# Optimization experiments

Hardware: AMD Instinct MI355X
Metric: run time of the kernel (lower is better)

## Reference

```python
import jax, jax.numpy as jnp
import numpy as np

N_NODES = 50000
N_EDGES = 800000
IN_FEATS = 64
HIDDEN = 64
NUM_CLASSES = 32


def _graph_conv(x, src, dst, W, b, n_nodes):
    # DGL GraphConv, norm='both', allow_zero_in_degree=True:
    # out = D_in^{-1/2} * (A^T @ (D_out^{-1/2} * x)) @ W + b, degrees clamped to >=1
    e = src.shape[0]
    ones = jnp.ones((e,), dtype=x.dtype)
    out_deg = jax.ops.segment_sum(ones, src, num_segments=n_nodes)
    in_deg = jax.ops.segment_sum(ones, dst, num_segments=n_nodes)
    norm_src = jax.lax.rsqrt(jnp.maximum(out_deg, 1.0))[:, None]
    norm_dst = jax.lax.rsqrt(jnp.maximum(in_deg, 1.0))[:, None]
    h = x * norm_src                                   # [N, d]
    agg = jax.ops.segment_sum(h[src], dst, num_segments=n_nodes)  # gather+scatter over edges
    return (agg * norm_dst) @ W + b


def setup_inputs() -> dict:
    key = jax.random.key(0)
    k1, k2, k3, k4, k5 = jax.random.split(key, 5)
    features = jax.random.normal(k1, (N_NODES, IN_FEATS), dtype=jnp.float32)
    src = jax.random.randint(k2, (N_EDGES,), 0, N_NODES, dtype=jnp.int32)
    dst = jax.random.randint(k3, (N_EDGES,), 0, N_NODES, dtype=jnp.int32)
    W1 = jax.random.normal(k4, (IN_FEATS, HIDDEN), dtype=jnp.float32) * (1.0 / np.sqrt(IN_FEATS))
    b1 = jnp.zeros((HIDDEN,), dtype=jnp.float32)
    W2 = jax.random.normal(k5, (HIDDEN, NUM_CLASSES), dtype=jnp.float32) * (1.0 / np.sqrt(HIDDEN))
    b2 = jnp.zeros((NUM_CLASSES,), dtype=jnp.float32)
    return {"features": features, "src": src, "dst": dst,
            "W1": W1, "b1": b1, "W2": W2, "b2": b2}


def reference(features, src, dst, W1, b1, W2, b2) -> jnp.ndarray:
    n = features.shape[0]
    h = jax.nn.relu(_graph_conv(features, src, dst, W1, b1, n))
    out = _graph_conv(h, src, dst, W2, b2, n)
    # single canonical etype -> mean over one-element stack is identity
    return out
```

## Files before the change

kernel.cpp:

```cpp
#include <hip/hip_runtime.h>
#include <hip/hip_bf16.h>

#define N_NODES 50000
#define N_EDGES 800000
#define F 64
#define C 32
#define CAP 48

#define NPB   800
#define EPB   1000
#define NBUCK 196
#define SEGCAP 5120

#define G1_BLOCKS   2048
#define GOUT_BLOCKS 2048
#define GY_BLOCKS   2048

static __device__ __forceinline__ float bflo(int u) {
    return __uint_as_float(((unsigned)u) << 16);
}
static __device__ __forceinline__ float bfhi(int u) {
    return __uint_as_float(((unsigned)u) & 0xffff0000u);
}
static __device__ __forceinline__ unsigned short f2bf(float f) {
    __hip_bfloat16 h = __float2bfloat16(f);
    return *reinterpret_cast<unsigned short*>(&h);
}

__global__ void part_fused_kernel(const int* __restrict__ src, const int* __restrict__ dst,
                                  int* __restrict__ gseg,
                                  int* __restrict__ edge_d, unsigned char* __restrict__ edge_s) {
    __shared__ int hd[4][NBUCK], hs[4][NBUCK];
    int t = threadIdx.x;
    int w = t >> 6;
    for (int i = t; i < 4 * NBUCK; i += 256) {
        (&hd[0][0])[i] = 0;
        (&hs[0][0])[i] = 0;
    }
    __syncthreads();
    int b0 = blockIdx.x * EPB;
    const int4* s4 = reinterpret_cast<const int4*>(src + b0);
    const int4* d4 = reinterpret_cast<const int4*>(dst + b0);
    for (int i = t; i < EPB / 4; i += 256) {
        int4 dv = d4[i];
        int4 sv = s4[i];
        atomicAdd(&hd[w][dv.x >> 8], 1); atomicAdd(&hd[w][dv.y >> 8], 1);
        atomicAdd(&hd[w][dv.z >> 8], 1); atomicAdd(&hd[w][dv.w >> 8], 1);
        atomicAdd(&hs[w][sv.x >> 8], 1); atomicAdd(&hs[w][sv.y >> 8], 1);
        atomicAdd(&hs[w][sv.z >> 8], 1); atomicAdd(&hs[w][sv.w >> 8], 1);
    }
    __syncthreads();
    if (t < NBUCK) {
        int c0 = hd[0][t], c1 = hd[1][t], c2 = hd[2][t], c3 = hd[3][t];
        int base = t * SEGCAP + atomicAdd(&gseg[t], c0 + c1 + c2 + c3);
        hd[0][t] = base;
        hd[1][t] = base + c0;
        hd[2][t] = base + c0 + c1;
        hd[3][t] = base + c0 + c1 + c2;
        c0 = hs[0][t]; c1 = hs[1][t]; c2 = hs[2][t]; c3 = hs[3][t];
        base = t * SEGCAP + atomicAdd(&gseg[NBUCK + t], c0 + c1 + c2 + c3);
        hs[0][t] = base;
        hs[1][t] = base + c0;
        hs[2][t] = base + c0 + c1;
        hs[3][t] = base + c0 + c1 + c2;
    }
    __syncthreads();
    for (int i = t; i < EPB / 4; i += 256) {
        int4 dv = d4[i];
        int4 sv = s4[i];
        int p;
        p = atomicAdd(&hd[w][dv.x >> 8], 1); edge_d[p] = ((dv.x & 255) << 16) | sv.x;
        p = atomicAdd(&hd[w][dv.y >> 8], 1); edge_d[p] = ((dv.y & 255) << 16) | sv.y;
        p = atomicAdd(&hd[w][dv.z >> 8], 1); edge_d[p] = ((dv.z & 255) << 16) | sv.z;
        p = atomicAdd(&hd[w][dv.w >> 8], 1); edge_d[p] = ((dv.w & 255) << 16) | sv.w;
        p = atomicAdd(&hs[w][sv.x >> 8], 1); edge_s[p] = (unsigned char)(sv.x & 255);
        p = atomicAdd(&hs[w][sv.y >> 8], 1); edge_s[p] = (unsigned char)(sv.y & 255);
        p = atomicAdd(&hs[w][sv.z >> 8], 1); edge_s[p] = (unsigned char)(sv.z & 255);
        p = atomicAdd(&hs[w][sv.w >> 8], 1); edge_s[p] = (unsigned char)(sv.w & 255);
    }
}

__global__ void bucket_build_kernel(const int* __restrict__ edge_d,
                                    const unsigned char* __restrict__ edge_s,
                                    const int* __restrict__ gseg,
                                    unsigned short* __restrict__ csr,
                                    float4* __restrict__ meta) {
    __shared__ int cur[256];
    __shared__ int hsm[256];
    int t = threadIdx.x;
    int bucket = blockIdx.x;
    cur[t] = 0;
    hsm[t] = 0;
    __syncthreads();
    int lend = gseg[bucket];           if (lend > SEGCAP) lend = SEGCAP;
    int lens = gseg[NBUCK + bucket];   if (lens > SEGCAP) lens = SEGCAP;
    int lo = bucket * SEGCAP;
    for (int i = lo + t; i < lo + lend; i += 256) {
        int pd = edge_d[i];
        int dlow = pd >> 16;
        int s = pd & 0xFFFF;
        int pos = atomicAdd(&cur[dlow], 1);
        if (pos < CAP)
            csr[(size_t)(bucket * 256 + dlow) * CAP + pos] = (unsigned short)s;
    }
    for (int i = lo + t; i < lo + lens; i += 256) {
        atomicAdd(&hsm[edge_s[i]], 1);
    }
    __syncthreads();
    int node = bucket * 256 + t;
    if (node < N_NODES) {
        int c = cur[t] < CAP ? cur[t] : CAP;
        float4 m;
        m.x = rsqrtf(fmaxf((float)c, 1.0f));
        m.y = rsqrtf(fmaxf((float)hsm[t], 1.0f));
        m.z = __int_as_float(c);
        m.w = 0.f;
        meta[node] = m;
    }
}

__global__ void gemm_y_kernel(const float* __restrict__ x,
                              const float4* __restrict__ meta,
                              const float* __restrict__ W,
                              __hip_bfloat16* __restrict__ y) {
    __shared__ float sW[F * F];
    __shared__ float srow[16][F];
    int t = threadIdx.x;
    for (int i = t; i < F * F; i += 256) sW[i] = W[i];
    int j = t & 63;
    int w = t >> 6;
    for (int tile = blockIdx.x; tile < N_NODES / 16; tile += GY_BLOCKS) {
        int base = tile * 16;
        __syncthreads();
        for (int r = w; r < 16; r += 4) srow[r][j] = x[(size_t)(base + r) * F + j];
        __syncthreads();
        float a0 = 0, a1 = 0, a2 = 0, a3 = 0;
#pragma unroll
        for (int k = 0; k < F; k++) {
            float wv = sW[k * F + j];
            a0 += srow[w * 4 + 0][k] * wv;
            a1 += srow[w * 4 + 1][k] * wv;
            a2 += srow[w * 4 + 2][k] * wv;
            a3 += srow[w * 4 + 3][k] * wv;
        }
        int n0 = base + w * 4;
        y[(size_t)(n0 + 0) * F + j] = __float2bfloat16(a0 * meta[n0 + 0].y);
        y[(size_t)(n0 + 1) * F + j] = __float2bfloat16(a1 * meta[n0 + 1].y);
        y[(size_t)(n0 + 2) * F + j] = __float2bfloat16(a2 * meta[n0 + 2].y);
        y[(size_t)(n0 + 3) * F + j] = __float2bfloat16(a3 * meta[n0 + 3].y);
    }
}

__global__ void gather64_gemv_kernel(const __hip_bfloat16* __restrict__ y,
                                     const unsigned short* __restrict__ csr,
                                     const float4* __restrict__ meta,
                                     const float* __restrict__ b1,
                                     const float* __restrict__ W2,
                                     __hip_bfloat16* __restrict__ gt) {
    __shared__ float sW[F * C];
    int t = threadIdx.x;
    for (int i = t; i < F * C; i += 256) sW[i] = W2[i];
    __syncthreads();
    int w    = t >> 6;
    int lane = t & 63;
    int g  = lane >> 3;
    int fo = (lane & 7) * 8;
    int j    = lane & 31;
    int half = lane >> 5;
    const float4 b1a = *reinterpret_cast<const float4*>(b1 + fo);
    const float4 b1b = *reinterpret_cast<const float4*>(b1 + fo + 4);
    const unsigned short* ytab = reinterpret_cast<const unsigned short*>(y);
    const int STRIDE = G1_BLOCKS * 4;

    int node = blockIdx.x * 4 + w;
    float4 pm = meta[node];
    const unsigned short* prow = csr + (size_t)node * CAP;
    int pr0 = prow[g], pr1 = prow[8 + g], pr2 = prow[16 + g];

    while (node < N_NODES) {
        float nd = pm.x, ns = pm.y;
        int n = __float_as_int(pm.z);
        int r0 = pr0, r1 = pr1, r2 = pr2;
        int nxt = node + STRIDE;
        int pf = (nxt < N_NODES) ? nxt : node;

        int ss0 = (g      < n) ? r0 : 0;  float m0 = (g      < n) ? 1.f : 0.f;
        int ss1 = (8  + g < n) ? r1 : 0;  float m1 = (8  + g < n) ? 1.f : 0.f;
        int ss2 = (16 + g < n) ? r2 : 0;  float m2 = (16 + g < n) ? 1.f : 0.f;

        const int4 v0 = *reinterpret_cast<const int4*>(ytab + (size_t)ss0 * F + fo);
        const int4 v1 = *reinterpret_cast<const int4*>(ytab + (size_t)ss1 * F + fo);
        const int4 v2 = *reinterpret_cast<const int4*>(ytab + (size_t)ss2 * F + fo);

        pm = meta[pf];
        const unsigned short* nrow = csr + (size_t)pf * CAP;
        pr0 = nrow[g]; pr1 = nrow[8 + g]; pr2 = nrow[16 + g];

        float a0, a1, a2, a3, a4, a5, a6, a7;
        a0 = m0 * bflo(v0.x); a1 = m0 * bfhi(v0.x);
        a2 = m0 * bflo(v0.y); a3 = m0 * bfhi(v0.y);
        a4 = m0 * bflo(v0.z); a5 = m0 * bfhi(v0.z);
        a6 = m0 * bflo(v0.w); a7 = m0 * bfhi(v0.w);

#define G1_ACC(vv, mm)                                                        \
        a0 = fmaf(mm, bflo(vv.x), a0); a1 = fmaf(mm, bfhi(vv.x), a1);         \
        a2 = fmaf(mm, bflo(vv.y), a2); a3 = fmaf(mm, bfhi(vv.y), a3);         \
        a4 = fmaf(mm, bflo(vv.z), a4); a5 = fmaf(mm, bfhi(vv.z), a5);         \
        a6 = fmaf(mm, bflo(vv.w), a6); a7 = fmaf(mm, bfhi(vv.w), a7);
        G1_ACC(v1, m1)
        G1_ACC(v2, m2)

        if (__builtin_expect(n > 24, 0)) {
            const unsigned short* row = csr + (size_t)node * CAP;
            int r3 = row[24 + g], r4 = row[32 + g], r5 = row[40 + g];
            int ss3 = (24 + g < n) ? r3 : 0;  float m3 = (24 + g < n) ? 1.f : 0.f;
            int ss4 = (32 + g < n) ? r4 : 0;  float m4 = (32 + g < n) ? 1.f : 0.f;
            int ss5 = (40 + g < n) ? r5 : 0;  float m5 = (40 + g < n) ? 1.f : 0.f;
            const int4 v3 = *reinterpret_cast<const int4*>(ytab + (size_t)ss3 * F + fo);
            const int4 v4 = *reinterpret_cast<const int4*>(ytab + (size_t)ss4 * F + fo);
            const int4 v5 = *reinterpret_cast<const int4*>(ytab + (size_t)ss5 * F + fo);
            G1_ACC(v3, m3)
            G1_ACC(v4, m4)
            G1_ACC(v5, m5)
        }
#undef G1_ACC

#define G1_RED(mk)                                                           \
        a0 += __shfl_xor(a0, mk); a1 += __shfl_xor(a1, mk);                  \
        a2 += __shfl_xor(a2, mk); a3 += __shfl_xor(a3, mk);                  \
        a4 += __shfl_xor(a4, mk); a5 += __shfl_xor(a5, mk);                  \
        a6 += __shfl_xor(a6, mk); a7 += __shfl_xor(a7, mk);
        G1_RED(8)
        G1_RED(16)
        G1_RED(32)
#undef G1_RED

        float hh[8];
        hh[0] = fmaxf(fmaf(a0, nd, b1a.x), 0.f) * ns;
        hh[1] = fmaxf(fmaf(a1, nd, b1a.y), 0.f) * ns;
        hh[2] = fmaxf(fmaf(a2, nd, b1a.z), 0.f) * ns;
        hh[3] = fmaxf(fmaf(a3, nd, b1a.w), 0.f) * ns;
        hh[4] = fmaxf(fmaf(a4, nd, b1b.x), 0.f) * ns;
        hh[5] = fmaxf(fmaf(a5, nd, b1b.y), 0.f) * ns;
        hh[6] = fmaxf(fmaf(a6, nd, b1b.z), 0.f) * ns;
        hh[7] = fmaxf(fmaf(a7, nd, b1b.w), 0.f) * ns;

        float o = 0.f;
#pragma unroll
        for (int k = 0; k < 32; k++) {
            float hv = __shfl(hh[k & 7], (half << 2) + (k >> 3));
            o = fmaf(hv, sW[(half * 32 + k) * C + j], o);
        }
        o += __shfl_down(o, 32);
        if (half == 0)
            __builtin_nontemporal_store(f2bf(o),
                reinterpret_cast<unsigned short*>(gt) + (size_t)node * C + j);
        node = nxt;
    }
}

__global__ void gather_out_kernel(const __hip_bfloat16* __restrict__ gt,
                                  const unsigned short* __restrict__ csr,
                                  const float4* __restrict__ meta,
                                  const float* __restrict__ b2,
                                  float* __restrict__ out) {
    int t = threadIdx.x;
    int w = t >> 6;
    int lane = t & 63;
    int g  = lane >> 3;
    int fo = (lane & 7) * 4;
    const unsigned short* tab = reinterpret_cast<const unsigned short*>(gt);
    const float4 bb = *reinterpret_cast<const float4*>(b2 + fo);
    const int STRIDE = GOUT_BLOCKS * 4;

    int node = blockIdx.x * 4 + w;
    float4 pm = meta[node];
    const unsigned short* prow = csr + (size_t)node * CAP;
    int pr0 = prow[g], pr1 = prow[8 + g], pr2 = prow[16 + g];

    while (node < N_NODES) {
        float nd = pm.x;
        int n = __float_as_int(pm.z);
        int r0 = pr0, r1 = pr1, r2 = pr2;
        int nxt = node + STRIDE;
        int pf = (nxt < N_NODES) ? nxt : node;

        int ss0 = (g      < n) ? r0 : 0;  float m0 = (g      < n) ? 1.f : 0.f;
        int ss1 = (8  + g < n) ? r1 : 0;  float m1 = (8  + g < n) ? 1.f : 0.f;
        int ss2 = (16 + g < n) ? r2 : 0;  float m2 = (16 + g < n) ? 1.f : 0.f;

        const int2 v0 = *reinterpret_cast<const int2*>(tab + (size_t)ss0 * C + fo);
        const int2 v1 = *reinterpret_cast<const int2*>(tab + (size_t)ss1 * C + fo);
        const int2 v2 = *reinterpret_cast<const int2*>(tab + (size_t)ss2 * C + fo);

        pm = meta[pf];
        const unsigned short* nrow = csr + (size_t)pf * CAP;
        pr0 = nrow[g]; pr1 = nrow[8 + g]; pr2 = nrow[16 + g];

        float a0, a1, a2, a3;
        a0 = m0 * bflo(v0.x); a1 = m0 * bfhi(v0.x);
        a2 = m0 * bflo(v0.y); a3 = m0 * bfhi(v0.y);

#define G2_ACC(vv, mm)                                                        \
        a0 = fmaf(mm, bflo(vv.x), a0); a1 = fmaf(mm, bfhi(vv.x), a1);         \
        a2 = fmaf(mm, bflo(vv.y), a2); a3 = fmaf(mm, bfhi(vv.y), a3);
        G2_ACC(v1, m1)
        G2_ACC(v2, m2)

        if (__builtin_expect(n > 24, 0)) {
            const unsigned short* row = csr + (size_t)node * CAP;
            int r3 = row[24 + g], r4 = row[32 + g], r5 = row[40 + g];
            int ss3 = (24 + g < n) ? r3 : 0;  float m3 = (24 + g < n) ? 1.f : 0.f;
            int ss4 = (32 + g < n) ? r4 : 0;  float m4 = (32 + g < n) ? 1.f : 0.f;
            int ss5 = (40 + g < n) ? r5 : 0;  float m5 = (40 + g < n) ? 1.f : 0.f;
            const int2 v3 = *reinterpret_cast<const int2*>(tab + (size_t)ss3 * C + fo);
            const int2 v4 = *reinterpret_cast<const int2*>(tab + (size_t)ss4 * C + fo);
            const int2 v5 = *reinterpret_cast<const int2*>(tab + (size_t)ss5 * C + fo);
            G2_ACC(v3, m3)
            G2_ACC(v4, m4)
            G2_ACC(v5, m5)
        }
#undef G2_ACC

        a0 += __shfl_xor(a0, 8);  a1 += __shfl_xor(a1, 8);
        a2 += __shfl_xor(a2, 8);  a3 += __shfl_xor(a3, 8);
        a0 += __shfl_xor(a0, 16); a1 += __shfl_xor(a1, 16);
        a2 += __shfl_xor(a2, 16); a3 += __shfl_xor(a3, 16);
        a0 += __shfl_xor(a0, 32); a1 += __shfl_xor(a1, 32);
        a2 += __shfl_xor(a2, 32); a3 += __shfl_xor(a3, 32);

        if (lane < 8) {
            float o0 = fmaf(a0, nd, bb.x);
            float o1 = fmaf(a1, nd, bb.y);
            float o2 = fmaf(a2, nd, bb.z);
            float o3 = fmaf(a3, nd, bb.w);
            unsigned long long p0 = ((unsigned long long)__float_as_uint(o0)) |
                                    ((unsigned long long)__float_as_uint(o1) << 32);
            unsigned long long p1 = ((unsigned long long)__float_as_uint(o2)) |
                                    ((unsigned long long)__float_as_uint(o3) << 32);
            unsigned long long* po = reinterpret_cast<unsigned long long*>(
                out + (size_t)node * C + fo);
            __builtin_nontemporal_store(p0, po);
            __builtin_nontemporal_store(p1, po + 1);
        }
        node = nxt;
    }
}

extern "C" void kernel_launch(void* const* d_in, const int* in_sizes, int n_in,
                              void* d_out, int out_size, void* d_ws, size_t ws_size,
                              hipStream_t stream) {
    const float* features = (const float*)d_in[0];
    const int*   src      = (const int*)d_in[1];
    const int*   dst      = (const int*)d_in[2];
    const float* W1       = (const float*)d_in[3];
    const float* b1       = (const float*)d_in[4];
    const float* W2       = (const float*)d_in[5];
    const float* b2       = (const float*)d_in[6];
    float* out = (float*)d_out;

    char* p = (char*)d_ws;
    float4* meta = (float4*)p;            p += (size_t)N_NODES * 16;
    unsigned short* csr = (unsigned short*)p; p += (size_t)N_NODES * CAP * 2;
    __hip_bfloat16* y  = (__hip_bfloat16*)p;  p += (size_t)N_NODES * F * 2;
    __hip_bfloat16* gt = (__hip_bfloat16*)p;

    int* edge_d = (int*)y;
    unsigned char* edge_s = (unsigned char*)(edge_d + NBUCK * SEGCAP);
    int* gseg   = (int*)gt;

    hipMemsetAsync(gseg, 0, (size_t)(2 * NBUCK) * 4, stream);

    part_fused_kernel<<<NPB, 256, 0, stream>>>(src, dst, gseg, edge_d, edge_s);
    bucket_build_kernel<<<NBUCK, 256, 0, stream>>>(edge_d, edge_s, gseg, csr, meta);

    gemm_y_kernel<<<GY_BLOCKS, 256, 0, stream>>>(features, meta, W1, y);
    gather64_gemv_kernel<<<G1_BLOCKS, 256, 0, stream>>>(y, csr, meta, b1, W2, gt);

    gather_out_kernel<<<GOUT_BLOCKS, 256, 0, stream>>>(gt, csr, meta, b2, out);
}
```

Baseline: 189.9 us.

## Fuse first-layer feature GEMM into bucket build kernel with 1024-thread blocks

Merges the X·W1 GEMM (scaled by source-degree norm) into the bucket/CSR build kernel, so each 1024-thread block builds its bucket's CSR and then computes y for the same 256 nodes in four passes. This removes one kernel launch and the meta reload, but the GEMM now runs on only 196 blocks instead of 2048. Edge staging buffers move to dedicated workspace because y is now written while edge_d is still being read. The result is less parallelism for the GEMM and a larger shared-memory footprint per block.

```diff
diff --git a/kernel.cpp b/kernel.cpp
--- a/kernel.cpp
+++ b/kernel.cpp
@@ -14,7 +14,6 @@
 
 #define G1_BLOCKS   2048
 #define GOUT_BLOCKS 2048
-#define GY_BLOCKS   2048
 
 static __device__ __forceinline__ float bflo(int u) {
     return __uint_as_float(((unsigned)u) << 16);
@@ -80,22 +79,29 @@
     }
 }
 
-__global__ void bucket_build_kernel(const int* __restrict__ edge_d,
-                                    const unsigned char* __restrict__ edge_s,
-                                    const int* __restrict__ gseg,
-                                    unsigned short* __restrict__ csr,
-                                    float4* __restrict__ meta) {
+__global__ void __launch_bounds__(1024)
+bucket_build_kernel(const int* __restrict__ edge_d,
+                    const unsigned char* __restrict__ edge_s,
+                    const int* __restrict__ gseg,
+                    const float* __restrict__ x,
+                    const float* __restrict__ W,
+                    unsigned short* __restrict__ csr,
+                    float4* __restrict__ meta,
+                    __hip_bfloat16* __restrict__ y) {
     __shared__ int cur[256];
     __shared__ int hsm[256];
+    __shared__ float nsb[256];
+    __shared__ float sW[F * F];
+    __shared__ float srow[64][F];
     int t = threadIdx.x;
     int bucket = blockIdx.x;
-    cur[t] = 0;
-    hsm[t] = 0;
+    if (t < 256) { cur[t] = 0; hsm[t] = 0; }
+    for (int i = t; i < F * F; i += 1024) sW[i] = W[i];
     __syncthreads();
     int lend = gseg[bucket];           if (lend > SEGCAP) lend = SEGCAP;
     int lens = gseg[NBUCK + bucket];   if (lens > SEGCAP) lens = SEGCAP;
     int lo = bucket * SEGCAP;
-    for (int i = lo + t; i < lo + lend; i += 256) {
+    for (int i = lo + t; i < lo + lend; i += 1024) {
         int pd = edge_d[i];
         int dlow = pd >> 16;
         int s = pd & 0xFFFF;
@@ -103,36 +109,36 @@
         if (pos < CAP)
             csr[(size_t)(bucket * 256 + dlow) * CAP + pos] = (unsigned short)s;
     }
-    for (int i = lo + t; i < lo + lens; i += 256) {
+    for (int i = lo + t; i < lo + lens; i += 1024) {
         atomicAdd(&hsm[edge_s[i]], 1);
     }
     __syncthreads();
-    int node = bucket * 256 + t;
-    if (node < N_NODES) {
-        int c = cur[t] < CAP ? cur[t] : CAP;
-        float4 m;
-        m.x = rsqrtf(fmaxf((float)c, 1.0f));
-        m.y = rsqrtf(fmaxf((float)hsm[t], 1.0f));
-        m.z = __int_as_float(c);
-        m.w = 0.f;
-        meta[node] = m;
-    }
-}
-
-__global__ void gemm_y_kernel(const float* __restrict__ x,
-                              const float4* __restrict__ meta,
-                              const float* __restrict__ W,
-                              __hip_bfloat16* __restrict__ y) {
-    __shared__ float sW[F * F];
-    __shared__ float srow[16][F];
-    int t = threadIdx.x;
-    for (int i = t; i < F * F; i += 256) sW[i] = W[i];
+    if (t < 256) {
+        int node = bucket * 256 + t;
+        if (node < N_NODES) {
+            int c = cur[t] < CAP ? cur[t] : CAP;
+            float ns = rsqrtf(fmaxf((float)hsm[t], 1.0f));
+            float4 m;
+            m.x = rsqrtf(fmaxf((float)c, 1.0f));
+            m.y = ns;
+            m.z = __int_as_float(c);
+            m.w = 0.f;
+            meta[node] = m;
+            nsb[t] = ns;
+        } else {
+            nsb[t] = 0.f;
+        }
+    }
+    __syncthreads();
+    int w = t >> 6;
     int j = t & 63;
-    int w = t >> 6;
-    for (int tile = blockIdx.x; tile < N_NODES / 16; tile += GY_BLOCKS) {
-        int base = tile * 16;
-        __syncthreads();
-        for (int r = w; r < 16; r += 4) srow[r][j] = x[(size_t)(base + r) * F + j];
+    for (int pass = 0; pass < 4; pass++) {
+        int base = bucket * 256 + pass * 64;
+        for (int idx = t; idx < 64 * F; idx += 1024) {
+            int r = idx >> 6;
+            int nn = base + r;
+            srow[r][idx & 63] = (nn < N_NODES) ? x[(size_t)nn * F + (idx & 63)] : 0.f;
+        }
         __syncthreads();
         float a0 = 0, a1 = 0, a2 = 0, a3 = 0;
 #pragma unroll
@@ -144,10 +150,19 @@
             a3 += srow[w * 4 + 3][k] * wv;
         }
         int n0 = base + w * 4;
-        y[(size_t)(n0 + 0) * F + j] = __float2bfloat16(a0 * meta[n0 + 0].y);
-        y[(size_t)(n0 + 1) * F + j] = __float2bfloat16(a1 * meta[n0 + 1].y);
-        y[(size_t)(n0 + 2) * F + j] = __float2bfloat16(a2 * meta[n0 + 2].y);
-        y[(size_t)(n0 + 3) * F + j] = __float2bfloat16(a3 * meta[n0 + 3].y);
+        int l0 = pass * 64 + w * 4;
+        if (n0 + 3 < N_NODES) {
+            y[(size_t)(n0 + 0) * F + j] = __float2bfloat16(a0 * nsb[l0 + 0]);
+            y[(size_t)(n0 + 1) * F + j] = __float2bfloat16(a1 * nsb[l0 + 1]);
+            y[(size_t)(n0 + 2) * F + j] = __float2bfloat16(a2 * nsb[l0 + 2]);
+            y[(size_t)(n0 + 3) * F + j] = __float2bfloat16(a3 * nsb[l0 + 3]);
+        } else {
+            if (n0 + 0 < N_NODES) y[(size_t)(n0 + 0) * F + j] = __float2bfloat16(a0 * nsb[l0 + 0]);
+            if (n0 + 1 < N_NODES) y[(size_t)(n0 + 1) * F + j] = __float2bfloat16(a1 * nsb[l0 + 1]);
+            if (n0 + 2 < N_NODES) y[(size_t)(n0 + 2) * F + j] = __float2bfloat16(a2 * nsb[l0 + 2]);
+            if (n0 + 3 < N_NODES) y[(size_t)(n0 + 3) * F + j] = __float2bfloat16(a3 * nsb[l0 + 3]);
+        }
+        __syncthreads();
     }
 }
 
@@ -363,18 +378,17 @@
     float4* meta = (float4*)p;            p += (size_t)N_NODES * 16;
     unsigned short* csr = (unsigned short*)p; p += (size_t)N_NODES * CAP * 2;
     __hip_bfloat16* y  = (__hip_bfloat16*)p;  p += (size_t)N_NODES * F * 2;
-    __hip_bfloat16* gt = (__hip_bfloat16*)p;
-
-    int* edge_d = (int*)y;
-    unsigned char* edge_s = (unsigned char*)(edge_d + NBUCK * SEGCAP);
-    int* gseg   = (int*)gt;
+    __hip_bfloat16* gt = (__hip_bfloat16*)p;  p += (size_t)N_NODES * C * 2;
+    int* edge_d = (int*)p;                p += (size_t)NBUCK * SEGCAP * 4;
+    unsigned char* edge_s = (unsigned char*)p; p += (size_t)NBUCK * SEGCAP;
+    int* gseg = (int*)p;
 
     hipMemsetAsync(gseg, 0, (size_t)(2 * NBUCK) * 4, stream);
 
     part_fused_kernel<<<NPB, 256, 0, stream>>>(src, dst, gseg, edge_d, edge_s);
-    bucket_build_kernel<<<NBUCK, 256, 0, stream>>>(edge_d, edge_s, gseg, csr, meta);
-
-    gemm_y_kernel<<<GY_BLOCKS, 256, 0, stream>>>(features, meta, W1, y);
+    bucket_build_kernel<<<NBUCK, 1024, 0, stream>>>(edge_d, edge_s, gseg,
+                                                    features, W1, csr, meta, y);
+
     gather64_gemv_kernel<<<G1_BLOCKS, 256, 0, stream>>>(y, csr, meta, b1, W2, gt);
 
     gather_out_kernel<<<GOUT_BLOCKS, 256, 0, stream>>>(gt, csr, meta, b2, out);
```

New measurement: 186.0 us (median of 2 runs). -2.0%, faster.
